# Optimization experiments

Measured on AMD Instinct MI355X. Metric: run time of the kernel, lower is better.

## Reference

```python
import jax, jax.numpy as jnp
import numpy as np

B, L, D = 1, 4096, 2048
H, KV, HD = 16, 4, 128
WINDOW = 1024
ROPE_BASE = 10000.0


def _rms_norm(x, scale):
    var = jnp.mean(jnp.square(x), axis=-1, keepdims=True)
    return x * jax.lax.rsqrt(var + 1e-6) * scale


def _apply_rope(x, positions, base_frequency):
    # x: (B, L, N, HD); positions: (B, L)
    head_dim = x.shape[-1]
    half = head_dim // 2
    freq_exp = 2.0 * jnp.arange(half, dtype=jnp.float32) / head_dim
    timescale = base_frequency ** freq_exp                       # (half,)
    sinusoid = positions[..., None].astype(jnp.float32) / timescale  # (B, L, half)
    sin = jnp.sin(sinusoid)[:, :, None, :]                       # (B, L, 1, half)
    cos = jnp.cos(sinusoid)[:, :, None, :]
    x1, x2 = x[..., :half], x[..., half:]
    return jnp.concatenate([x1 * cos - x2 * sin, x2 * cos + x1 * sin], axis=-1)


def setup_inputs() -> dict:
    key = jax.random.key(0)
    ks = jax.random.split(key, 5)
    x = jax.random.normal(ks[0], (B, L, D), dtype=jnp.float32)
    positions = jnp.broadcast_to(jnp.arange(L, dtype=jnp.int32), (B, L))
    s = D ** -0.5
    Wq = jax.random.normal(ks[1], (D, H * HD), dtype=jnp.float32) * s
    Wk = jax.random.normal(ks[2], (D, KV * HD), dtype=jnp.float32) * s
    Wv = jax.random.normal(ks[3], (D, KV * HD), dtype=jnp.float32) * s
    Wo = jax.random.normal(ks[4], (H * HD, D), dtype=jnp.float32) * ((H * HD) ** -0.5)
    q_scale = jnp.ones((HD,), dtype=jnp.float32)
    k_scale = jnp.ones((HD,), dtype=jnp.float32)
    return {"x": x, "positions": positions, "Wq": Wq, "Wk": Wk, "Wv": Wv,
            "Wo": Wo, "q_scale": q_scale, "k_scale": k_scale}


def reference(x, positions, Wq, Wk, Wv, Wo, q_scale, k_scale):
    q = (x @ Wq).reshape(B, L, H, HD)
    k = (x @ Wk).reshape(B, L, KV, HD)
    v = (x @ Wv).reshape(B, L, KV, HD)

    q = _apply_rope(_rms_norm(q, q_scale), positions, ROPE_BASE)
    k = _apply_rope(_rms_norm(k, k_scale), positions, ROPE_BASE)

    rep = H // KV
    k = jnp.repeat(k, rep, axis=2)   # (B, L, H, HD)
    v = jnp.repeat(v, rep, axis=2)

    scale = HD ** -0.5
    scores = jnp.einsum('bqhd,bkhd->bhqk', q, k) * scale  # (B, H, L, L)

    idx = jnp.arange(L)
    causal = idx[:, None] >= idx[None, :]
    window = idx[None, :] >= idx[:, None] - (WINDOW - 1)
    mask = causal & window
    scores = jnp.where(mask[None, None, :, :], scores, jnp.finfo(scores.dtype).min)
    attn = jax.nn.softmax(scores, axis=-1)

    out = jnp.einsum('bhqk,bkhd->bqhd', attn, v).reshape(B, L, H * HD)
    return out @ Wo
```

## Files before the change

### kernel.cpp

```cpp
#include <hip/hip_runtime.h>
#include <cstdint>
#include <cstddef>

typedef unsigned short u16;
typedef __attribute__((ext_vector_type(4))) float  float4v;
typedef __attribute__((ext_vector_type(4))) int    int4v;
typedef __attribute__((ext_vector_type(8))) short  short8v;
typedef __attribute__((ext_vector_type(4))) short  short4v;

#define L_SEQ 4096
#define NH 16
#define NKV 4
#define WND 1024

static __device__ __forceinline__ u16 f2bf(float f) {
  union { float f; unsigned u; } v; v.f = f;
  unsigned r = (v.u + 0x7FFFu + ((v.u >> 16) & 1u)) >> 16;
  return (u16)r;
}
static __device__ __forceinline__ u16 f2bf_fast(float f) {
  union { float f; unsigned u; } v; v.f = f;
  return (u16)((v.u + 0x8000u) >> 16);
}
static __device__ __forceinline__ float bf2f(u16 b) {
  union { unsigned u; float f; } v; v.u = ((unsigned)b) << 16;
  return v.f;
}

__global__ __launch_bounds__(256) void k_cvt(const float* __restrict__ in,
                                             u16* __restrict__ out, int n4) {
  int i = blockIdx.x * 256 + threadIdx.x;
  if (i >= n4) return;
  float4v v = ((const float4v*)in)[i];
  short4v o;
  o[0] = (short)f2bf(v[0]); o[1] = (short)f2bf(v[1]);
  o[2] = (short)f2bf(v[2]); o[3] = (short)f2bf(v[3]);
  ((short4v*)out)[i] = o;
}

__global__ __launch_bounds__(256) void k_transpose64(const float* __restrict__ in,
                                                     u16* __restrict__ out,
                                                     int K, int N, int row_off) {
  __shared__ float tile[64][65];
  int n0 = blockIdx.x * 64, k0 = blockIdx.y * 64;
  int tx = threadIdx.x & 63, ty = threadIdx.x >> 6;
#pragma unroll
  for (int i = 0; i < 16; i++)
    tile[ty + i*4][tx] = in[(size_t)(k0 + ty + i*4)*N + n0 + tx];
  __syncthreads();
#pragma unroll
  for (int i = 0; i < 16; i++)
    out[(size_t)(row_off + n0 + ty + i*4)*K + k0 + tx] = f2bf(tile[tx][ty + i*4]);
}

__global__ __launch_bounds__(256) void k_vtrans(const u16* __restrict__ qkvb,
                                                u16* __restrict__ vT) {
  __shared__ u16 tile[64][66];
  int p0 = blockIdx.x * 64, d0 = blockIdx.y * 64;
  int tx = threadIdx.x & 63, ty = threadIdx.x >> 6;
#pragma unroll
  for (int i = 0; i < 16; i++)
    tile[ty + i*4][tx] = qkvb[(size_t)(p0 + ty + i*4)*3072 + 2560 + d0 + tx];
  __syncthreads();
#pragma unroll
  for (int i = 0; i < 16; i++)
    vT[(size_t)(d0 + ty + i*4)*L_SEQ + p0 + tx] = tile[tx][ty + i*4];
}

template<int BF16_OUT>
__global__ __launch_bounds__(256) void k_gemm_bt(const u16* __restrict__ A,
                                                 const u16* __restrict__ B,
                                                 void* __restrict__ Cv,
                                                 int M, int N, int K) {
  __shared__ alignas(16) u16 As[128*64];
  __shared__ alignas(16) u16 Bs[128*64];
  int tid = threadIdx.x;
  int lane = tid & 63, wave = tid >> 6;
  int lr = lane & 15, lg = lane >> 4;
  int m0 = blockIdx.y * 128, n0 = blockIdx.x * 128;
  int wm = (wave >> 1) * 64, wn = (wave & 1) * 64;

  float4v acc[4][4];
#pragma unroll
  for (int i = 0; i < 4; i++)
#pragma unroll
    for (int j = 0; j < 4; j++)
#pragma unroll
      for (int r = 0; r < 4; r++) acc[i][j][r] = 0.f;

  for (int kt = 0; kt < K; kt += 64) {
    __syncthreads();
#pragma unroll
    for (int it = 0; it < 4; it++) {
      int s = it*256 + tid;
      int row = s >> 3, j = s & 7;
      int col = ((j ^ (row & 7)) << 3);
      __builtin_amdgcn_global_load_lds(
          (const __attribute__((address_space(1))) void*)(A + (size_t)(m0 + row)*K + kt + col),
          (__attribute__((address_space(3))) void*)(&As[s * 8]), 16, 0, 0);
      __builtin_amdgcn_global_load_lds(
          (const __attribute__((address_space(1))) void*)(B + (size_t)(n0 + row)*K + kt + col),
          (__attribute__((address_space(3))) void*)(&Bs[s * 8]), 16, 0, 0);
    }
    __syncthreads();
#pragma unroll
    for (int half = 0; half < 2; half++) {
      short8v af[4], bf[4];
#pragma unroll
      for (int i = 0; i < 4; i++) {
        int row = wm + i*16 + lr;
        af[i] = *(const short8v*)(&As[row*64 + ((((half<<2)|lg) ^ (row & 7)) << 3)]);
      }
#pragma unroll
      for (int j = 0; j < 4; j++) {
        int row = wn + j*16 + lr;
        bf[j] = *(const short8v*)(&Bs[row*64 + ((((half<<2)|lg) ^ (row & 7)) << 3)]);
      }
#pragma unroll
      for (int i = 0; i < 4; i++)
#pragma unroll
        for (int j = 0; j < 4; j++)
          acc[i][j] = __builtin_amdgcn_mfma_f32_16x16x32_bf16(af[i], bf[j], acc[i][j], 0, 0, 0);
    }
  }
#pragma unroll
  for (int i = 0; i < 4; i++)
#pragma unroll
    for (int j = 0; j < 4; j++)
#pragma unroll
      for (int r = 0; r < 4; r++) {
        size_t idx = (size_t)(m0 + wm + i*16 + lg*4 + r)*N + (n0 + wn + j*16 + lr);
        if (BF16_OUT) ((u16*)Cv)[idx] = f2bf(acc[i][j][r]);
        else          ((float*)Cv)[idx] = acc[i][j][r];
      }
}

__global__ __launch_bounds__(256) void k_qknorm(const u16* __restrict__ qkvb,
    const int* __restrict__ positions, const float* __restrict__ q_scale,
    const float* __restrict__ k_scale, u16* __restrict__ qb,
    u16* __restrict__ kb) {
  int p = blockIdx.x * 4 + (threadIdx.x >> 6);
  int l = threadIdx.x & 63;
  const float LOG2_BASE = 13.287712379549449f;
  float ang = (float)positions[p] * exp2f(-(float)l * (LOG2_BASE / 64.0f));
  float sn, cs; sincosf(ang, &sn, &cs);
  float qs1 = q_scale[l], qs2 = q_scale[l + 64];
  float ks1 = k_scale[l], ks2 = k_scale[l + 64];
  const u16* base = qkvb + (size_t)p * 3072;
  const float qsc = 0.12751741505539613f;
#pragma unroll
  for (int h = 0; h < 16; h++) {
    float x1 = bf2f(base[h*128 + l]), x2 = bf2f(base[h*128 + l + 64]);
    float ss = x1*x1 + x2*x2;
#pragma unroll
    for (int m = 1; m < 64; m <<= 1) ss += __shfl_xor(ss, m);
    float rinv = rsqrtf(ss * (1.0f/128.0f) + 1e-6f);
    x1 *= rinv * qs1; x2 *= rinv * qs2;
    u16* dst = qb + ((size_t)p*NH + h)*128;
    dst[l]      = f2bf((x1*cs - x2*sn) * qsc);
    dst[l + 64] = f2bf((x2*cs + x1*sn) * qsc);
  }
#pragma unroll
  for (int g = 0; g < 4; g++) {
    float x1 = bf2f(base[2048 + g*128 + l]), x2 = bf2f(base[2048 + g*128 + l + 64]);
    float ss = x1*x1 + x2*x2;
#pragma unroll
    for (int m = 1; m < 64; m <<= 1) ss += __shfl_xor(ss, m);
    float rinv = rsqrtf(ss * (1.0f/128.0f) + 1e-6f);
    x1 *= rinv * ks1; x2 *= rinv * ks2;
    u16* dst = kb + ((size_t)p*NKV + g)*128;
    dst[l]      = f2bf(x1*cs - x2*sn);
    dst[l + 64] = f2bf(x2*cs + x1*sn);
  }
}

__global__ __launch_bounds__(256) void k_attn(const u16* __restrict__ qb,
    const u16* __restrict__ kb, const u16* __restrict__ vT,
    u16* __restrict__ ob) {
  __shared__ alignas(16) u16 Ks[64*128];
  __shared__ alignas(16) u16 Vs[128*64];
  __shared__ alignas(16) u16 Pw[4][2][16*72];
  int tid = threadIdx.x;
  int lane = tid & 63, wave = tid >> 6;
  int lr = lane & 15, lg = lane >> 4;
  int flat = blockIdx.x;
  int xcd = flat & 7, slot = flat >> 3;
  int gh = xcd >> 1;
  int q0 = ((xcd & 1) * 64 + slot) * 32;
  int h = gh * 4 + wave;

  short8v qf[2][4];
#pragma unroll
  for (int m = 0; m < 2; m++) {
    const u16* qrow = qb + ((size_t)(q0 + m*16 + lr)*NH + h)*128 + lg*8;
#pragma unroll
    for (int t = 0; t < 4; t++) qf[m][t] = *(const short8v*)(qrow + t*32);
  }

  const short one_bf = (short)0x3F80;
  const short8v ones = {one_bf,one_bf,one_bf,one_bf,one_bf,one_bf,one_bf,one_bf};

  float4v O[9][2];
#pragma unroll
  for (int dt = 0; dt < 9; dt++)
#pragma unroll
    for (int m = 0; m < 2; m++)
#pragma unroll
      for (int r = 0; r < 4; r++) O[dt][m][r] = 0.f;

  int kstart = q0 - (WND - 1); if (kstart < 0) kstart = 0; kstart &= ~63;
  for (int kt = kstart; kt < q0 + 32; kt += 64) {
    __syncthreads();
#pragma unroll
    for (int it = 0; it < 4; it++) {
      int s = it*256 + tid;
      { int row = s >> 4, j = s & 15, col = (j ^ (row & 15)) << 3;
        __builtin_amdgcn_global_load_lds(
            (const __attribute__((address_space(1))) void*)(kb + (size_t)(kt + row)*512 + gh*128 + col),
            (__attribute__((address_space(3))) void*)(&Ks[s * 8]), 16, 0, 0); }
      { int row = s >> 3, j = s & 7, col = (j ^ (row & 7)) << 3;
        __builtin_amdgcn_global_load_lds(
            (const __attribute__((address_space(1))) void*)(vT + (size_t)(gh*128 + row)*L_SEQ + kt + col),
            (__attribute__((address_space(3))) void*)(&Vs[s * 8]), 16, 0, 0); }
    }
    __syncthreads();

    float4v S[2][4];
#pragma unroll
    for (int m = 0; m < 2; m++)
#pragma unroll
      for (int t2 = 0; t2 < 4; t2++)
#pragma unroll
        for (int r = 0; r < 4; r++) S[m][t2][r] = 0.f;
#pragma unroll
    for (int t2 = 0; t2 < 4; t2++) {
      int row = t2*16 + lr;
#pragma unroll
      for (int t = 0; t < 4; t++) {
        short8v kf = *(const short8v*)(&Ks[row*128 + (((t*4 + lg) ^ (row & 15)) << 3)]);
        S[0][t2] = __builtin_amdgcn_mfma_f32_16x16x32_bf16(qf[0][t], kf, S[0][t2], 0, 0, 0);
        S[1][t2] = __builtin_amdgcn_mfma_f32_16x16x32_bf16(qf[1][t], kf, S[1][t2], 0, 0, 0);
      }
    }

    bool need_mask = (kt + 64 > q0) || (kt < q0 - (WND - 32));
    if (need_mask) {
#pragma unroll
      for (int m = 0; m < 2; m++)
#pragma unroll
        for (int r = 0; r < 4; r++) {
          int pos = q0 + m*16 + lg*4 + r;
#pragma unroll
          for (int t2 = 0; t2 < 4; t2++) {
            int key = kt + t2*16 + lr;
            float p = (key > pos || key < pos - (WND - 1)) ? 0.f : exp2f(S[m][t2][r]);
            Pw[wave][m][(lg*4 + r)*72 + t2*16 + lr] = f2bf_fast(p);
          }
        }
    } else {
#pragma unroll
      for (int m = 0; m < 2; m++)
#pragma unroll
        for (int r = 0; r < 4; r++)
#pragma unroll
          for (int t2 = 0; t2 < 4; t2++)
            Pw[wave][m][(lg*4 + r)*72 + t2*16 + lr] = f2bf_fast(exp2f(S[m][t2][r]));
    }

    short8v pf[2][2];
#pragma unroll
    for (int m = 0; m < 2; m++)
#pragma unroll
      for (int sub = 0; sub < 2; sub++)
        pf[m][sub] = *(const short8v*)(&Pw[wave][m][lr*72 + sub*32 + lg*8]);

#pragma unroll
    for (int sub = 0; sub < 2; sub++)
#pragma unroll
      for (int dt = 0; dt < 8; dt++) {
        int row = dt*16 + lr;
        short8v vf = *(const short8v*)(&Vs[row*64 + (((sub*4 + lg) ^ (row & 7)) << 3)]);
        O[dt][0] = __builtin_amdgcn_mfma_f32_16x16x32_bf16(pf[0][sub], vf, O[dt][0], 0, 0, 0);
        O[dt][1] = __builtin_amdgcn_mfma_f32_16x16x32_bf16(pf[1][sub], vf, O[dt][1], 0, 0, 0);
      }
#pragma unroll
    for (int m = 0; m < 2; m++) {
      O[8][m] = __builtin_amdgcn_mfma_f32_16x16x32_bf16(pf[m][0], ones, O[8][m], 0, 0, 0);
      O[8][m] = __builtin_amdgcn_mfma_f32_16x16x32_bf16(pf[m][1], ones, O[8][m], 0, 0, 0);
    }
  }

#pragma unroll
  for (int m = 0; m < 2; m++)
#pragma unroll
    for (int r = 0; r < 4; r++) {
      float inv = 1.0f / O[8][m][r];
#pragma unroll
      for (int dt = 0; dt < 8; dt++)
        ob[((size_t)(q0 + m*16 + lg*4 + r)*NH + h)*128 + dt*16 + lr] =
            f2bf(O[dt][m][r] * inv);
    }
}

extern "C" void kernel_launch(void* const* d_in, const int* in_sizes, int n_in,
                              void* d_out, int out_size, void* d_ws, size_t ws_size,
                              hipStream_t stream) {
  (void)in_sizes; (void)n_in; (void)out_size; (void)ws_size;
  const float* x        = (const float*)d_in[0];
  const int*   positions= (const int*)d_in[1];
  const float* Wq       = (const float*)d_in[2];
  const float* Wk       = (const float*)d_in[3];
  const float* Wv       = (const float*)d_in[4];
  const float* Wo       = (const float*)d_in[5];
  const float* q_scale  = (const float*)d_in[6];
  const float* k_scale  = (const float*)d_in[7];
  float* out = (float*)d_out;

  char* ws = (char*)d_ws;
  u16* xb   = (u16*)ws; ws += (size_t)4096*2048*2;
  u16* Wt   = (u16*)ws; ws += (size_t)3072*2048*2;
  u16* Wot  = (u16*)ws; ws += (size_t)2048*2048*2;
  u16* qkvb = (u16*)ws; ws += (size_t)4096*3072*2;
  u16* qb   = (u16*)ws; ws += (size_t)4096*2048*2;
  u16* kb   = (u16*)ws; ws += (size_t)4096*512*2;
  u16* vT   = (u16*)ws; ws += (size_t)4096*512*2;
  u16* ob   = qkvb;

  k_cvt<<<8192, 256, 0, stream>>>(x, xb, 2097152);
  k_transpose64<<<dim3(32,32), 256, 0, stream>>>(Wq, Wt, 2048, 2048, 0);
  k_transpose64<<<dim3(8,32),  256, 0, stream>>>(Wk, Wt, 2048, 512, 2048);
  k_transpose64<<<dim3(8,32),  256, 0, stream>>>(Wv, Wt, 2048, 512, 2560);
  k_transpose64<<<dim3(32,32), 256, 0, stream>>>(Wo, Wot, 2048, 2048, 0);
  k_gemm_bt<1><<<dim3(24,32), 256, 0, stream>>>(xb, Wt, qkvb, 4096, 3072, 2048);
  k_qknorm<<<1024, 256, 0, stream>>>(qkvb, positions, q_scale, k_scale, qb, kb);
  k_vtrans<<<dim3(64,8), 256, 0, stream>>>(qkvb, vT);
  k_attn<<<512, 256, 0, stream>>>(qb, kb, vT, ob);
  k_gemm_bt<0><<<dim3(16,32), 256, 0, stream>>>(ob, Wot, out, 4096, 2048, 2048);
}
```

Before: 288.9 us.

## Double-buffer K/V tiles with 32-key steps and interleave query-tile block mapping

Shrinks the attention key tile from 64 to 32 rows and double-buffers K and V in shared memory, so the next tile's global-to-LDS load is issued while the current tile is computed. It also changes the block-to-query-tile mapping so the two XCDs sharing a KV head group get interleaved 16-tile chunks, which balances the causal workload. The step count doubles and there is a single barrier per step. The smaller tiles also cut LDS use and the number of live S registers, at the cost of more loop iterations and less work per barrier.

```diff
diff --git a/kernel.cpp b/kernel.cpp
--- a/kernel.cpp
+++ b/kernel.cpp
@@ -177,16 +177,18 @@
 __global__ __launch_bounds__(256) void k_attn(const u16* __restrict__ qb,
     const u16* __restrict__ kb, const u16* __restrict__ vT,
     u16* __restrict__ ob) {
-  __shared__ alignas(16) u16 Ks[64*128];
-  __shared__ alignas(16) u16 Vs[128*64];
-  __shared__ alignas(16) u16 Pw[4][2][16*72];
+  __shared__ alignas(16) u16 Ks[2][32*128];
+  __shared__ alignas(16) u16 Vs[2][128*32];
+  __shared__ alignas(16) u16 Pw[4][2][16*40];
   int tid = threadIdx.x;
   int lane = tid & 63, wave = tid >> 6;
   int lr = lane & 15, lg = lane >> 4;
   int flat = blockIdx.x;
-  int xcd = flat & 7, slot = flat >> 3;
+  int xcd = flat & 7, s = flat >> 3;
   int gh = xcd >> 1;
-  int q0 = ((xcd & 1) * 64 + slot) * 32;
+  int chunk = s >> 4;
+  int qtile = (chunk*2 + (xcd & 1))*16 + (s & 15);
+  int q0 = qtile * 32;
   int h = gh * 4 + wave;
 
   short8v qf[2][4];
@@ -200,50 +202,59 @@
   const short one_bf = (short)0x3F80;
   const short8v ones = {one_bf,one_bf,one_bf,one_bf,one_bf,one_bf,one_bf,one_bf};
 
-  float4v O[9][2];
-#pragma unroll
-  for (int dt = 0; dt < 9; dt++)
+  float4v O[8][2], den[2];
+#pragma unroll
+  for (int dt = 0; dt < 8; dt++)
 #pragma unroll
     for (int m = 0; m < 2; m++)
 #pragma unroll
       for (int r = 0; r < 4; r++) O[dt][m][r] = 0.f;
-
-  int kstart = q0 - (WND - 1); if (kstart < 0) kstart = 0; kstart &= ~63;
-  for (int kt = kstart; kt < q0 + 32; kt += 64) {
-    __syncthreads();
-#pragma unroll
-    for (int it = 0; it < 4; it++) {
-      int s = it*256 + tid;
-      { int row = s >> 4, j = s & 15, col = (j ^ (row & 15)) << 3;
+#pragma unroll
+  for (int m = 0; m < 2; m++)
+#pragma unroll
+    for (int r = 0; r < 4; r++) den[m][r] = 0.f;
+
+  auto stage = [&](int buf, int kt) {
+#pragma unroll
+    for (int it = 0; it < 2; it++) {
+      int s2 = it*256 + tid;
+      { int row = s2 >> 4, j = s2 & 15, col = (j ^ (row & 15)) << 3;
         __builtin_amdgcn_global_load_lds(
             (const __attribute__((address_space(1))) void*)(kb + (size_t)(kt + row)*512 + gh*128 + col),
-            (__attribute__((address_space(3))) void*)(&Ks[s * 8]), 16, 0, 0); }
-      { int row = s >> 3, j = s & 7, col = (j ^ (row & 7)) << 3;
+            (__attribute__((address_space(3))) void*)(&Ks[buf][s2 * 8]), 16, 0, 0); }
+      { int row = s2 >> 2, j = s2 & 3, col = (j ^ (row & 3)) << 3;
         __builtin_amdgcn_global_load_lds(
             (const __attribute__((address_space(1))) void*)(vT + (size_t)(gh*128 + row)*L_SEQ + kt + col),
-            (__attribute__((address_space(3))) void*)(&Vs[s * 8]), 16, 0, 0); }
-    }
+            (__attribute__((address_space(3))) void*)(&Vs[buf][s2 * 8]), 16, 0, 0); }
+    }
+  };
+
+  int kstart = q0 - (WND - 1); if (kstart < 0) kstart = 0; kstart &= ~31;
+  stage(0, kstart);
+  int cur = 0;
+  for (int kt = kstart; kt < q0 + 32; kt += 32) {
     __syncthreads();
-
-    float4v S[2][4];
+    if (kt + 32 < q0 + 32) stage(cur ^ 1, kt + 32);
+
+    float4v S[2][2];
 #pragma unroll
     for (int m = 0; m < 2; m++)
 #pragma unroll
-      for (int t2 = 0; t2 < 4; t2++)
+      for (int t2 = 0; t2 < 2; t2++)
 #pragma unroll
         for (int r = 0; r < 4; r++) S[m][t2][r] = 0.f;
 #pragma unroll
-    for (int t2 = 0; t2 < 4; t2++) {
+    for (int t2 = 0; t2 < 2; t2++) {
       int row = t2*16 + lr;
 #pragma unroll
       for (int t = 0; t < 4; t++) {
-        short8v kf = *(const short8v*)(&Ks[row*128 + (((t*4 + lg) ^ (row & 15)) << 3)]);
+        short8v kf = *(const short8v*)(&Ks[cur][row*128 + (((t*4 + lg) ^ (row & 15)) << 3)]);
         S[0][t2] = __builtin_amdgcn_mfma_f32_16x16x32_bf16(qf[0][t], kf, S[0][t2], 0, 0, 0);
         S[1][t2] = __builtin_amdgcn_mfma_f32_16x16x32_bf16(qf[1][t], kf, S[1][t2], 0, 0, 0);
       }
     }
 
-    bool need_mask = (kt + 64 > q0) || (kt < q0 - (WND - 32));
+    bool need_mask = (kt + 32 > q0) || (kt < q0 - (WND - 32));
     if (need_mask) {
 #pragma unroll
       for (int m = 0; m < 2; m++)
@@ -251,10 +262,10 @@
         for (int r = 0; r < 4; r++) {
           int pos = q0 + m*16 + lg*4 + r;
 #pragma unroll
-          for (int t2 = 0; t2 < 4; t2++) {
+          for (int t2 = 0; t2 < 2; t2++) {
             int key = kt + t2*16 + lr;
             float p = (key > pos || key < pos - (WND - 1)) ? 0.f : exp2f(S[m][t2][r]);
-            Pw[wave][m][(lg*4 + r)*72 + t2*16 + lr] = f2bf_fast(p);
+            Pw[wave][m][(lg*4 + r)*40 + t2*16 + lr] = f2bf_fast(p);
           }
         }
     } else {
@@ -263,38 +274,32 @@
 #pragma unroll
         for (int r = 0; r < 4; r++)
 #pragma unroll
-          for (int t2 = 0; t2 < 4; t2++)
-            Pw[wave][m][(lg*4 + r)*72 + t2*16 + lr] = f2bf_fast(exp2f(S[m][t2][r]));
-    }
-
-    short8v pf[2][2];
+          for (int t2 = 0; t2 < 2; t2++)
+            Pw[wave][m][(lg*4 + r)*40 + t2*16 + lr] = f2bf_fast(exp2f(S[m][t2][r]));
+    }
+
+    short8v pf[2];
 #pragma unroll
     for (int m = 0; m < 2; m++)
-#pragma unroll
-      for (int sub = 0; sub < 2; sub++)
-        pf[m][sub] = *(const short8v*)(&Pw[wave][m][lr*72 + sub*32 + lg*8]);
-
-#pragma unroll
-    for (int sub = 0; sub < 2; sub++)
-#pragma unroll
-      for (int dt = 0; dt < 8; dt++) {
-        int row = dt*16 + lr;
-        short8v vf = *(const short8v*)(&Vs[row*64 + (((sub*4 + lg) ^ (row & 7)) << 3)]);
-        O[dt][0] = __builtin_amdgcn_mfma_f32_16x16x32_bf16(pf[0][sub], vf, O[dt][0], 0, 0, 0);
-        O[dt][1] = __builtin_amdgcn_mfma_f32_16x16x32_bf16(pf[1][sub], vf, O[dt][1], 0, 0, 0);
-      }
-#pragma unroll
-    for (int m = 0; m < 2; m++) {
-      O[8][m] = __builtin_amdgcn_mfma_f32_16x16x32_bf16(pf[m][0], ones, O[8][m], 0, 0, 0);
-      O[8][m] = __builtin_amdgcn_mfma_f32_16x16x32_bf16(pf[m][1], ones, O[8][m], 0, 0, 0);
-    }
+      pf[m] = *(const short8v*)(&Pw[wave][m][lr*40 + lg*8]);
+
+#pragma unroll
+    for (int dt = 0; dt < 8; dt++) {
+      int row = dt*16 + lr;
+      short8v vf = *(const short8v*)(&Vs[cur][row*32 + ((lg ^ (row & 3)) << 3)]);
+      O[dt][0] = __builtin_amdgcn_mfma_f32_16x16x32_bf16(pf[0], vf, O[dt][0], 0, 0, 0);
+      O[dt][1] = __builtin_amdgcn_mfma_f32_16x16x32_bf16(pf[1], vf, O[dt][1], 0, 0, 0);
+    }
+    den[0] = __builtin_amdgcn_mfma_f32_16x16x32_bf16(pf[0], ones, den[0], 0, 0, 0);
+    den[1] = __builtin_amdgcn_mfma_f32_16x16x32_bf16(pf[1], ones, den[1], 0, 0, 0);
+    cur ^= 1;
   }
 
 #pragma unroll
   for (int m = 0; m < 2; m++)
 #pragma unroll
     for (int r = 0; r < 4; r++) {
-      float inv = 1.0f / O[8][m][r];
+      float inv = 1.0f / den[m][r];
 #pragma unroll
       for (int dt = 0; dt < 8; dt++)
         ob[((size_t)(q0 + m*16 + lg*4 + r)*NH + h)*128 + dt*16 + lr] =
```

Measured after the change: 301.7 us. 4.4% more time.
